# Kernel tuning notes

Hardware: AMD Instinct MI355X
Metric: run time of the kernel (lower is better)

The kernel has to match this reference:

```python
import jax, jax.numpy as jnp
import numpy as np
import math

BS, N_AGENTS, TOPK = 256, 64, 8
IN_DIM, HID, ATT, N_ACT = 128, 256, 64, 16


def setup_inputs() -> dict:
    key = jax.random.key(0)
    ks = jax.random.split(key, 20)
    s = 0.05
    return {
        "inputs": jax.random.normal(ks[0], (BS * N_AGENTS, IN_DIM), jnp.float32),
        "hidden_state": jax.random.normal(ks[1], (BS * N_AGENTS, HID), jnp.float32),
        "msg": jax.random.normal(ks[2], (BS * N_AGENTS, HID), jnp.float32),
        "topk_indices": jax.random.randint(ks[3], (BS, N_AGENTS, TOPK), 0, N_AGENTS, jnp.int32),
        "fc1_w": jax.random.normal(ks[4], (HID, IN_DIM), jnp.float32) * s,
        "fc1_b": jnp.zeros((HID,), jnp.float32),
        "gru_w_ih": jax.random.normal(ks[5], (3 * HID, HID), jnp.float32) * s,
        "gru_b_ih": jnp.zeros((3 * HID,), jnp.float32),
        "gru_w_hh": jax.random.normal(ks[6], (3 * HID, HID), jnp.float32) * s,
        "gru_b_hh": jnp.zeros((3 * HID,), jnp.float32),
        "q_w": jax.random.normal(ks[7], (ATT, HID), jnp.float32) * s,
        "q_b": jnp.zeros((ATT,), jnp.float32),
        "k_w": jax.random.normal(ks[8], (ATT, HID), jnp.float32) * s,
        "k_b": jnp.zeros((ATT,), jnp.float32),
        "v_w": jax.random.normal(ks[9], (HID, HID), jnp.float32) * s,
        "v_b": jnp.zeros((HID,), jnp.float32),
        "fc2a_w": jax.random.normal(ks[10], (HID, 2 * HID), jnp.float32) * s,
        "fc2a_b": jnp.zeros((HID,), jnp.float32),
        "fc2b_w": jax.random.normal(ks[11], (N_ACT, HID), jnp.float32) * s,
        "fc2b_b": jnp.zeros((N_ACT,), jnp.float32),
    }


def _forward(inputs, hidden_state, msg, topk_indices,
             fc1_w, fc1_b, gru_w_ih, gru_b_ih, gru_w_hh, gru_b_hh,
             q_w, q_b, k_w, k_b, v_w, v_b, fc2a_w, fc2a_b, fc2b_w, fc2b_b):
    # fc1 + ReLU
    x = jax.nn.relu(inputs @ fc1_w.T + fc1_b)  # [B*N, HID]
    # GRUCell (torch semantics)
    gi = x @ gru_w_ih.T + gru_b_ih             # [B*N, 3H]
    gh = hidden_state @ gru_w_hh.T + gru_b_hh
    i_r, i_z, i_n = jnp.split(gi, 3, axis=-1)
    h_r, h_z, h_n = jnp.split(gh, 3, axis=-1)
    r = jax.nn.sigmoid(i_r + h_r)
    z = jax.nn.sigmoid(i_z + h_z)
    n = jnp.tanh(i_n + r * h_n)
    h = (1.0 - z) * n + z * hidden_state       # [B*N, HID]

    # communicate: gather top-k neighbor messages, attend, aggregate
    msg_r = msg.reshape(BS, N_AGENTS, HID)
    msg_received = jax.vmap(lambda m, idx: m[idx])(msg_r, topk_indices)  # [B,N,K,HID]
    ego_h = h.reshape(BS, N_AGENTS, HID)
    q = ego_h @ q_w.T + q_b                    # [B,N,ATT]
    k = msg_received @ k_w.T + k_b             # [B,N,K,ATT]
    logits = jnp.einsum('bnka,bna->bnk', k, q) / math.sqrt(ATT)
    attn = jax.nn.softmax(logits, axis=-1)     # [B,N,K]
    m = msg_received @ v_w.T + v_b             # [B,N,K,HID]
    m_agg = jnp.einsum('bnk,bnkh->bnh', attn, m).reshape(BS * N_AGENTS, HID)

    out = jnp.concatenate([h, m_agg], axis=-1)  # [B*N, 2H]
    q_out = jax.nn.relu(out @ fc2a_w.T + fc2a_b) @ fc2b_w.T + fc2b_b  # [B*N, N_ACT]
    return q_out, h, m_agg


def reference(inputs, hidden_state, msg, topk_indices,
              fc1_w, fc1_b, gru_w_ih, gru_b_ih, gru_w_hh, gru_b_hh,
              q_w, q_b, k_w, k_b, v_w, v_b, fc2a_w, fc2a_b, fc2b_w, fc2b_b):
    return _forward(inputs, hidden_state, msg, topk_indices,
                    fc1_w, fc1_b, gru_w_ih, gru_b_ih, gru_w_hh, gru_b_hh,
                    q_w, q_b, k_w, k_b, v_w, v_b, fc2a_w, fc2a_b, fc2b_w, fc2b_b)
```

## Files before the change

### kernel.cpp

```cpp
#include <hip/hip_runtime.h>

typedef __bf16 bf16;
typedef __attribute__((ext_vector_type(8))) __bf16 bf16x8;
typedef __attribute__((ext_vector_type(4))) __bf16 bf16x4;
typedef __attribute__((ext_vector_type(4))) float f32x4;

static constexpr int ROWS = 16384;

static constexpr size_t OFF_WFC1 = 0;
static constexpr size_t OFF_WRX  = 32768;
static constexpr size_t OFF_WZX  = 98304;
static constexpr size_t OFF_WNI  = 163840;
static constexpr size_t OFF_WRH  = 229376;
static constexpr size_t OFF_WZH  = 294912;
static constexpr size_t OFF_WNH  = 360448;
static constexpr size_t OFF_WQ   = 425984;
static constexpr size_t OFF_WKV  = 442368;
static constexpr size_t OFF_F2AH = 524288;
static constexpr size_t OFF_F2AM = 589824;
static constexpr size_t OFF_WF2B = 655360;
static constexpr size_t OFF_INSW = 659456;

struct SwzSeg { const float* src; bf16* dst; int items; int k8s; int k32; int ld; };
struct SwzArgs { SwzSeg seg[14]; int count; };

__global__ __launch_bounds__(256) void swz_k(SwzArgs a) {
    const int tid = blockIdx.x * 256 + threadIdx.x;
    const int stride = gridDim.x * 256;
    for (int s = 0; s < a.count; ++s) {
        const float* __restrict__ src = a.seg[s].src;
        bf16* __restrict__ dst = a.seg[s].dst;
        const int items = a.seg[s].items, k8s = a.seg[s].k8s;
        const int k32c = a.seg[s].k32, ld = a.seg[s].ld;
        for (int i = tid; i < items; i += stride) {
            const int n = i >> k8s, kb = i & ((1 << k8s) - 1);
            const int k0 = kb << 3;
            const int lane = (n & 15) | ((kb & 3) << 4);
            const size_t off = ((size_t)((n >> 4) * k32c + (kb >> 2)) * 64 + lane) * 8;
            const float* p = src + (size_t)n * ld + k0;
            float4 f0 = *(const float4*)p;
            float4 f1 = *(const float4*)(p + 4);
            bf16x8 o = { (bf16)f0.x, (bf16)f0.y, (bf16)f0.z, (bf16)f0.w,
                         (bf16)f1.x, (bf16)f1.y, (bf16)f1.z, (bf16)f1.w };
            *(bf16x8*)(dst + off) = o;
        }
    }
}

template<int FM, int FN, int K32>
__device__ __forceinline__ void mm_swz(f32x4 (&acc)[FM][FN],
    const bf16* __restrict__ sA, int lda,
    const bf16* __restrict__ W, int lane)
{
    const int lr = lane & 15, lk = (lane >> 4) << 3;
    #pragma unroll
    for (int k32 = 0; k32 < K32; ++k32) {
        bf16x8 a[FM], b[FN];
        #pragma unroll
        for (int j = 0; j < FN; ++j)
            b[j] = *(const bf16x8*)(W + ((size_t)(j * K32 + k32) * 64 + lane) * 8);
        #pragma unroll
        for (int i = 0; i < FM; ++i)
            a[i] = *(const bf16x8*)&sA[(i * 16 + lr) * lda + k32 * 32 + lk];
        #pragma unroll
        for (int i = 0; i < FM; ++i)
            #pragma unroll
            for (int j = 0; j < FN; ++j)
                acc[i][j] = __builtin_amdgcn_mfma_f32_16x16x32_bf16(a[i], b[j], acc[i][j], 0, 0, 0);
    }
}

template<int FM, int FN, int K32>
__device__ __forceinline__ void mm_gg(f32x4 (&acc)[FM][FN],
    const bf16* __restrict__ A, const bf16* __restrict__ W, int lane)
{
    #pragma unroll
    for (int k32 = 0; k32 < K32; ++k32) {
        bf16x8 a[FM], b[FN];
        #pragma unroll
        for (int i = 0; i < FM; ++i)
            a[i] = *(const bf16x8*)(A + ((size_t)(i * K32 + k32) * 64 + lane) * 8);
        #pragma unroll
        for (int j = 0; j < FN; ++j)
            b[j] = *(const bf16x8*)(W + ((size_t)(j * K32 + k32) * 64 + lane) * 8);
        #pragma unroll
        for (int i = 0; i < FM; ++i)
            #pragma unroll
            for (int j = 0; j < FN; ++j)
                acc[i][j] = __builtin_amdgcn_mfma_f32_16x16x32_bf16(a[i], b[j], acc[i][j], 0, 0, 0);
    }
}

__device__ __forceinline__ float sigmf(float x) { return 1.f / (1.f + __expf(-x)); }
__device__ __forceinline__ float tanh_fast(float x) {
    x = fminf(fmaxf(x, -15.f), 15.f);
    float e2 = __expf(2.f * x);
    return (e2 - 1.f) / (e2 + 1.f);
}

__global__ __launch_bounds__(1024)
void mega_k(const bf16* __restrict__ insw, const float* __restrict__ hid_f,
            const float* __restrict__ msg_f, const int* __restrict__ topk,
            const bf16* __restrict__ Wfc1, const float* __restrict__ fc1_b,
            const bf16* __restrict__ WrX, const bf16* __restrict__ WrH,
            const bf16* __restrict__ WzX, const bf16* __restrict__ WzH,
            const bf16* __restrict__ Wni, const bf16* __restrict__ Wnh,
            const float* __restrict__ b_ih, const float* __restrict__ b_hh,
            const bf16* __restrict__ Wq, const float* __restrict__ q_b,
            const bf16* __restrict__ Wkv, const float* __restrict__ v_bias,
            const bf16* __restrict__ f2aH, const bf16* __restrict__ f2aM,
            const float* __restrict__ f2a_b,
            const bf16* __restrict__ Wf2b, const float* __restrict__ f2b_b,
            float* __restrict__ h_out, float* __restrict__ magg_out,
            float* __restrict__ q_out)
{
    __shared__ bf16 sH[64 * 264];
    __shared__ bf16 sB[64 * 264];
    __shared__ bf16 sG[64 * 264];
    __shared__ bf16 sM[64 * 264];
    __shared__ bf16 sQ[64 * 72];
    __shared__ bf16 sK[64 * 72];
    __shared__ int  sIdx[512];
    const int tid = threadIdx.x;
    const int wave = tid >> 6, lane = tid & 63;
    const int b64 = blockIdx.x * 64;
    const int lr = lane & 15, l4 = (lane >> 4) << 2, lk = (lane >> 4) << 3;

    #pragma unroll
    for (int c = tid; c < 4096; c += 1024) {
        int r = c >> 6, cg = (c & 63) << 2;
        float4 f = *(const float4*)(hid_f + (size_t)(b64 + r) * 256 + cg);
        float4 g = *(const float4*)(msg_f + (size_t)(b64 + r) * 256 + cg);
        bf16x4 oh = { (bf16)f.x, (bf16)f.y, (bf16)f.z, (bf16)f.w };
        bf16x4 og = { (bf16)g.x, (bf16)g.y, (bf16)g.z, (bf16)g.w };
        *(bf16x4*)&sH[r * 264 + cg] = oh;
        *(bf16x4*)&sG[r * 264 + cg] = og;
    }
    if (tid < 512) sIdx[tid] = topk[(size_t)blockIdx.x * 512 + tid];

    {
        f32x4 fa[1][4] = {};
        mm_gg<1, 4, 4>(fa, insw + (size_t)(blockIdx.x * 4 + (wave & 3)) * 4 * 512,
                       Wfc1 + (size_t)((wave >> 2) * 4) * 4 * 512, lane);
        #pragma unroll
        for (int j = 0; j < 4; ++j) {
            const int col = (wave >> 2) * 64 + j * 16 + lr;
            const float bv = fc1_b[col];
            #pragma unroll
            for (int rr = 0; rr < 4; ++rr)
                sB[((wave & 3) * 16 + l4 + rr) * 264 + col] = (bf16)fmaxf(fa[0][j][rr] + bv, 0.f);
        }
    }
    __syncthreads();

    f32x4 rg[4] = {}, zg[4] = {}, ng[4] = {}, hg[4] = {};
    {
        const size_t nb = (size_t)wave * 8 * 512;
        const bf16 *pRX = WrX + nb, *pZX = WzX + nb, *pNI = Wni + nb;
        const bf16 *pRH = WrH + nb, *pZH = WzH + nb, *pNH = Wnh + nb;
        #pragma unroll
        for (int k32 = 0; k32 < 8; ++k32) {
            const size_t bo = (size_t)k32 * 512 + lane * 8;
            bf16x8 brx = *(const bf16x8*)(pRX + bo);
            bf16x8 bzx = *(const bf16x8*)(pZX + bo);
            bf16x8 bni = *(const bf16x8*)(pNI + bo);
            bf16x8 brh = *(const bf16x8*)(pRH + bo);
            bf16x8 bzh = *(const bf16x8*)(pZH + bo);
            bf16x8 bnh = *(const bf16x8*)(pNH + bo);
            #pragma unroll
            for (int i = 0; i < 4; ++i) {
                bf16x8 ax = *(const bf16x8*)&sB[(i * 16 + lr) * 264 + k32 * 32 + lk];
                rg[i] = __builtin_amdgcn_mfma_f32_16x16x32_bf16(ax, brx, rg[i], 0, 0, 0);
                zg[i] = __builtin_amdgcn_mfma_f32_16x16x32_bf16(ax, bzx, zg[i], 0, 0, 0);
                ng[i] = __builtin_amdgcn_mfma_f32_16x16x32_bf16(ax, bni, ng[i], 0, 0, 0);
            }
            #pragma unroll
            for (int i = 0; i < 4; ++i) {
                bf16x8 ah = *(const bf16x8*)&sH[(i * 16 + lr) * 264 + k32 * 32 + lk];
                rg[i] = __builtin_amdgcn_mfma_f32_16x16x32_bf16(ah, brh, rg[i], 0, 0, 0);
                zg[i] = __builtin_amdgcn_mfma_f32_16x16x32_bf16(ah, bzh, zg[i], 0, 0, 0);
                hg[i] = __builtin_amdgcn_mfma_f32_16x16x32_bf16(ah, bnh, hg[i], 0, 0, 0);
            }
        }
    }
    {
        const int col = wave * 16 + lr;
        const float br = b_ih[col] + b_hh[col];
        const float bz = b_ih[256 + col] + b_hh[256 + col];
        const float bi = b_ih[512 + col], bh = b_hh[512 + col];
        #pragma unroll
        for (int i = 0; i < 4; ++i)
            #pragma unroll
            for (int rr = 0; rr < 4; ++rr) {
                const int row = i * 16 + l4 + rr;
                const float rv = sigmf(rg[i][rr] + br);
                const float zv = sigmf(zg[i][rr] + bz);
                const float nn = tanh_fast((ng[i][rr] + bi) + rv * (hg[i][rr] + bh));
                const float hd = (float)sH[row * 264 + col];
                const float h = (1.f - zv) * nn + zv * hd;
                h_out[(size_t)(b64 + row) * 256 + col] = h;
                sM[row * 264 + col] = (bf16)h;
            }
    }
    __syncthreads();

    if (wave < 4) {
        f32x4 a[4][2] = {};
        mm_swz<4, 2, 8>(a, sG, 264, Wkv + (size_t)(wave * 2) * 8 * 512, lane);
        #pragma unroll
        for (int i = 0; i < 4; ++i)
            #pragma unroll
            for (int j = 0; j < 2; ++j) {
                const int col = (wave * 2 + j) * 16 + lr;
                #pragma unroll
                for (int rr = 0; rr < 4; ++rr) {
                    const int row = i * 16 + l4 + rr;
                    if (col < 64) sK[row * 72 + col] = (bf16)a[i][j][rr];
                    else          sB[row * 264 + col - 64] = (bf16)a[i][j][rr];
                }
            }
    } else {
        f32x4 a[4][1] = {};
        mm_swz<4, 1, 8>(a, sG, 264, Wkv + (size_t)(4 + wave) * 8 * 512, lane);
        const int col = (4 + wave) * 16 + lr;
        #pragma unroll
        for (int i = 0; i < 4; ++i)
            #pragma unroll
            for (int rr = 0; rr < 4; ++rr)
                sB[(i * 16 + l4 + rr) * 264 + col - 64] = (bf16)a[i][0][rr];
    }
    {
        f32x4 qa[1][1] = {};
        mm_swz<1, 1, 8>(qa, sM + (wave & 3) * 16 * 264, 264,
                        Wq + (size_t)(wave >> 2) * 8 * 512, lane);
        const int col = (wave >> 2) * 16 + lr;
        const float bv = q_b[col];
        #pragma unroll
        for (int rr = 0; rr < 4; ++rr)
            sQ[((wave & 3) * 16 + l4 + rr) * 72 + col] = (bf16)(qa[0][0][rr] + bv);
    }
    __syncthreads();

    const int kk = lane >> 3, dg = lane & 7;
    #pragma unroll
    for (int uu = 0; uu < 4; ++uu) {
        const int u = wave * 4 + uu;
        const int rowk = sIdx[u * 8 + kk];
        bf16x8 q8 = *(const bf16x8*)&sQ[u * 72 + dg * 8];
        bf16x8 k8 = *(const bf16x8*)&sK[rowk * 72 + dg * 8];
        float s = 0.f;
        #pragma unroll
        for (int t = 0; t < 8; ++t) s += (float)q8[t] * (float)k8[t];
        s += __shfl_xor(s, 1); s += __shfl_xor(s, 2); s += __shfl_xor(s, 4);
        float logit = s * 0.125f;
        float mx = logit;
        mx = fmaxf(mx, __shfl_xor(mx, 8));
        mx = fmaxf(mx, __shfl_xor(mx, 16));
        mx = fmaxf(mx, __shfl_xor(mx, 32));
        float e = __expf(logit - mx);
        float den = e;
        den += __shfl_xor(den, 8); den += __shfl_xor(den, 16); den += __shfl_xor(den, 32);
        const float wv = e / den;
        float a0 = 0.f, a1 = 0.f, a2 = 0.f, a3 = 0.f;
        #pragma unroll
        for (int k = 0; k < 8; ++k) {
            float wk = __shfl(wv, k * 8);
            int   rk = __shfl(rowk, k * 8);
            bf16x4 v = *(const bf16x4*)&sB[rk * 264 + lane * 4];
            a0 += wk * (float)v[0]; a1 += wk * (float)v[1];
            a2 += wk * (float)v[2]; a3 += wk * (float)v[3];
        }
        float4 vb = *(const float4*)(v_bias + lane * 4);
        a0 += vb.x; a1 += vb.y; a2 += vb.z; a3 += vb.w;
        float4 res = { a0, a1, a2, a3 };
        *(float4*)(magg_out + (size_t)(b64 + u) * 256 + lane * 4) = res;
        bf16x4 rb = { (bf16)a0, (bf16)a1, (bf16)a2, (bf16)a3 };
        *(bf16x4*)&sH[u * 264 + lane * 4] = rb;
    }
    __syncthreads();

    {
        const int wm = wave >> 3, wn = wave & 7;
        f32x4 acc[2][2] = {};
        mm_swz<2, 2, 8>(acc, sM + wm * 32 * 264, 264, f2aH + (size_t)(wn * 2) * 8 * 512, lane);
        mm_swz<2, 2, 8>(acc, sH + wm * 32 * 264, 264, f2aM + (size_t)(wn * 2) * 8 * 512, lane);
        #pragma unroll
        for (int i = 0; i < 2; ++i)
            #pragma unroll
            for (int j = 0; j < 2; ++j) {
                const int col = wn * 32 + j * 16 + lr;
                const float bv = f2a_b[col];
                #pragma unroll
                for (int rr = 0; rr < 4; ++rr)
                    sG[(wm * 32 + i * 16 + l4 + rr) * 264 + col] = (bf16)fmaxf(acc[i][j][rr] + bv, 0.f);
            }
    }
    __syncthreads();

    if (wave < 4) {
        f32x4 acc[1][1] = {};
        mm_swz<1, 1, 8>(acc, sG + wave * 16 * 264, 264, Wf2b, lane);
        const float bv = f2b_b[lr];
        #pragma unroll
        for (int rr = 0; rr < 4; ++rr)
            q_out[(size_t)(b64 + wave * 16 + l4 + rr) * 16 + lr] = acc[0][0][rr] + bv;
    }
}

extern "C" void kernel_launch(void* const* d_in, const int* in_sizes, int n_in,
                              void* d_out, int out_size, void* d_ws, size_t ws_size,
                              hipStream_t stream)
{
    const float* in_f   = (const float*)d_in[0];
    const float* hid_f  = (const float*)d_in[1];
    const float* msg_f  = (const float*)d_in[2];
    const int*   topk   = (const int*)d_in[3];
    const float* fc1w_f = (const float*)d_in[4];
    const float* fc1_b  = (const float*)d_in[5];
    const float* wih_f  = (const float*)d_in[6];
    const float* b_ih   = (const float*)d_in[7];
    const float* whh_f  = (const float*)d_in[8];
    const float* b_hh   = (const float*)d_in[9];
    const float* qw_f   = (const float*)d_in[10];
    const float* q_b    = (const float*)d_in[11];
    const float* kw_f   = (const float*)d_in[12];
    const float* vw_f   = (const float*)d_in[14];
    const float* v_b    = (const float*)d_in[15];
    const float* f2aw_f = (const float*)d_in[16];
    const float* f2a_b  = (const float*)d_in[17];
    const float* f2bw_f = (const float*)d_in[18];
    const float* f2b_b  = (const float*)d_in[19];

    bf16* ws = (bf16*)d_ws;
    bf16* Wfc1 = ws + OFF_WFC1;
    bf16* WrX  = ws + OFF_WRX;
    bf16* WzX  = ws + OFF_WZX;
    bf16* Wni  = ws + OFF_WNI;
    bf16* WrH  = ws + OFF_WRH;
    bf16* WzH  = ws + OFF_WZH;
    bf16* Wnh  = ws + OFF_WNH;
    bf16* Wq   = ws + OFF_WQ;
    bf16* Wkv  = ws + OFF_WKV;
    bf16* f2aH = ws + OFF_F2AH;
    bf16* f2aM = ws + OFF_F2AM;
    bf16* Wf2b = ws + OFF_WF2B;
    bf16* insw = ws + OFF_INSW;

    float* q_out    = (float*)d_out;
    float* h_out    = q_out + (size_t)ROWS * 16;
    float* magg_out = h_out + (size_t)ROWS * 256;

    SwzArgs sa{};
    int s = 0;
    auto add = [&](const float* src, bf16* dst, int N, int K, int ld) {
        sa.seg[s].src = src; sa.seg[s].dst = dst;
        sa.seg[s].items = N * (K >> 3);
        sa.seg[s].k8s = (K == 128) ? 4 : 5;
        sa.seg[s].k32 = K >> 5;
        sa.seg[s].ld = ld; ++s;
    };
    add(fc1w_f,          Wfc1, 256, 128, 128);
    add(wih_f,           WrX,  256, 256, 256);
    add(wih_f +  65536,  WzX,  256, 256, 256);
    add(wih_f + 131072,  Wni,  256, 256, 256);
    add(whh_f,           WrH,  256, 256, 256);
    add(whh_f +  65536,  WzH,  256, 256, 256);
    add(whh_f + 131072,  Wnh,  256, 256, 256);
    add(qw_f,            Wq,    64, 256, 256);
    add(kw_f,            Wkv,   64, 256, 256);
    add(vw_f,            Wkv + 16384, 256, 256, 256);
    add(f2aw_f,          f2aH, 256, 256, 512);
    add(f2aw_f + 256,    f2aM, 256, 256, 512);
    add(f2bw_f,          Wf2b,  16, 256, 256);
    add(in_f,            insw, 16384, 128, 128);
    sa.count = s;
    swz_k<<<512, 256, 0, stream>>>(sa);

    mega_k<<<256, 1024, 0, stream>>>(insw, hid_f, msg_f, topk,
                                     Wfc1, fc1_b, WrX, WrH, WzX, WzH, Wni, Wnh,
                                     b_ih, b_hh, Wq, q_b, Wkv, v_b,
                                     f2aH, f2aM, f2a_b, Wf2b, f2b_b,
                                     h_out, magg_out, q_out);
}
```

Measured before the change: 56.46 us.

## Load fp32 inputs directly in fc1, drop input swizzle, prefetch weights in GEMMs

The fc1 stage now reads the fp32 input rows straight from global memory and converts them to bf16 in registers. This removes the swizzle pass over the 16384x128 input and its workspace round trip, and the swizzle kernel grid is halved. The GRU gate and fc2a GEMMs are restructured to software-prefetch the next k-slice of weight fragments while the current MFMAs run. fc2a also changes from a 2x2 wave tiling to one 16-column slice per wave over all 64 rows. In exchange, the fc1 A-fragment loads are uncoalesced strided fp32 reads, and fc2a now re-reads the LDS A tiles once per column slice.

```diff
diff --git a/kernel.cpp b/kernel.cpp
--- a/kernel.cpp
+++ b/kernel.cpp
@@ -19,7 +19,6 @@
 static constexpr size_t OFF_F2AH = 524288;
 static constexpr size_t OFF_F2AM = 589824;
 static constexpr size_t OFF_WF2B = 655360;
-static constexpr size_t OFF_INSW = 659456;
 
 struct SwzSeg { const float* src; bf16* dst; int items; int k8s; int k32; int ld; };
 struct SwzArgs { SwzSeg seg[14]; int count; };
@@ -70,24 +69,32 @@
     }
 }
 
-template<int FM, int FN, int K32>
-__device__ __forceinline__ void mm_gg(f32x4 (&acc)[FM][FN],
-    const bf16* __restrict__ A, const bf16* __restrict__ W, int lane)
+__device__ __forceinline__ void gate3(f32x4 (&g1)[4], f32x4 (&g2)[4], f32x4 (&g3)[4],
+    const bf16* __restrict__ sA,
+    const bf16* __restrict__ p1, const bf16* __restrict__ p2,
+    const bf16* __restrict__ p3, int lane)
 {
+    const int lr = lane & 15, lk = (lane >> 4) << 3;
+    const int lo = lane * 8;
+    bf16x8 c1 = *(const bf16x8*)(p1 + lo);
+    bf16x8 c2 = *(const bf16x8*)(p2 + lo);
+    bf16x8 c3 = *(const bf16x8*)(p3 + lo);
     #pragma unroll
-    for (int k32 = 0; k32 < K32; ++k32) {
-        bf16x8 a[FM], b[FN];
-        #pragma unroll
-        for (int i = 0; i < FM; ++i)
-            a[i] = *(const bf16x8*)(A + ((size_t)(i * K32 + k32) * 64 + lane) * 8);
-        #pragma unroll
-        for (int j = 0; j < FN; ++j)
-            b[j] = *(const bf16x8*)(W + ((size_t)(j * K32 + k32) * 64 + lane) * 8);
-        #pragma unroll
-        for (int i = 0; i < FM; ++i)
-            #pragma unroll
-            for (int j = 0; j < FN; ++j)
-                acc[i][j] = __builtin_amdgcn_mfma_f32_16x16x32_bf16(a[i], b[j], acc[i][j], 0, 0, 0);
+    for (int k = 0; k < 8; ++k) {
+        bf16x8 n1, n2, n3;
+        if (k < 7) {
+            n1 = *(const bf16x8*)(p1 + (k + 1) * 512 + lo);
+            n2 = *(const bf16x8*)(p2 + (k + 1) * 512 + lo);
+            n3 = *(const bf16x8*)(p3 + (k + 1) * 512 + lo);
+        }
+        #pragma unroll
+        for (int i = 0; i < 4; ++i) {
+            bf16x8 a = *(const bf16x8*)&sA[(i * 16 + lr) * 264 + k * 32 + lk];
+            g1[i] = __builtin_amdgcn_mfma_f32_16x16x32_bf16(a, c1, g1[i], 0, 0, 0);
+            g2[i] = __builtin_amdgcn_mfma_f32_16x16x32_bf16(a, c2, g2[i], 0, 0, 0);
+            g3[i] = __builtin_amdgcn_mfma_f32_16x16x32_bf16(a, c3, g3[i], 0, 0, 0);
+        }
+        if (k < 7) { c1 = n1; c2 = n2; c3 = n3; }
     }
 }
 
@@ -99,7 +106,7 @@
 }
 
 __global__ __launch_bounds__(1024)
-void mega_k(const bf16* __restrict__ insw, const float* __restrict__ hid_f,
+void mega_k(const float* __restrict__ in_f, const float* __restrict__ hid_f,
             const float* __restrict__ msg_f, const int* __restrict__ topk,
             const bf16* __restrict__ Wfc1, const float* __restrict__ fc1_b,
             const bf16* __restrict__ WrX, const bf16* __restrict__ WrH,
@@ -139,50 +146,37 @@
     if (tid < 512) sIdx[tid] = topk[(size_t)blockIdx.x * 512 + tid];
 
     {
-        f32x4 fa[1][4] = {};
-        mm_gg<1, 4, 4>(fa, insw + (size_t)(blockIdx.x * 4 + (wave & 3)) * 4 * 512,
-                       Wfc1 + (size_t)((wave >> 2) * 4) * 4 * 512, lane);
+        f32x4 fa[4] = {};
+        const float* ap = in_f + (size_t)(b64 + (wave & 3) * 16 + lr) * 128 + lk;
+        const bf16*  wp = Wfc1 + (size_t)(wave >> 2) * 16 * 512 + lane * 8;
+        #pragma unroll
+        for (int k = 0; k < 4; ++k) {
+            float4 f0 = *(const float4*)(ap + k * 32);
+            float4 f1 = *(const float4*)(ap + k * 32 + 4);
+            bf16x8 af = { (bf16)f0.x, (bf16)f0.y, (bf16)f0.z, (bf16)f0.w,
+                          (bf16)f1.x, (bf16)f1.y, (bf16)f1.z, (bf16)f1.w };
+            #pragma unroll
+            for (int j = 0; j < 4; ++j) {
+                bf16x8 bfr = *(const bf16x8*)(wp + (size_t)(j * 4 + k) * 512);
+                fa[j] = __builtin_amdgcn_mfma_f32_16x16x32_bf16(af, bfr, fa[j], 0, 0, 0);
+            }
+        }
         #pragma unroll
         for (int j = 0; j < 4; ++j) {
             const int col = (wave >> 2) * 64 + j * 16 + lr;
             const float bv = fc1_b[col];
             #pragma unroll
             for (int rr = 0; rr < 4; ++rr)
-                sB[((wave & 3) * 16 + l4 + rr) * 264 + col] = (bf16)fmaxf(fa[0][j][rr] + bv, 0.f);
-        }
-    }
-    __syncthreads();
-
+                sB[((wave & 3) * 16 + l4 + rr) * 264 + col] = (bf16)fmaxf(fa[j][rr] + bv, 0.f);
+        }
+    }
+    __syncthreads();
+
+    const size_t nb = (size_t)wave * 8 * 512;
     f32x4 rg[4] = {}, zg[4] = {}, ng[4] = {}, hg[4] = {};
-    {
-        const size_t nb = (size_t)wave * 8 * 512;
-        const bf16 *pRX = WrX + nb, *pZX = WzX + nb, *pNI = Wni + nb;
-        const bf16 *pRH = WrH + nb, *pZH = WzH + nb, *pNH = Wnh + nb;
-        #pragma unroll
-        for (int k32 = 0; k32 < 8; ++k32) {
-            const size_t bo = (size_t)k32 * 512 + lane * 8;
-            bf16x8 brx = *(const bf16x8*)(pRX + bo);
-            bf16x8 bzx = *(const bf16x8*)(pZX + bo);
-            bf16x8 bni = *(const bf16x8*)(pNI + bo);
-            bf16x8 brh = *(const bf16x8*)(pRH + bo);
-            bf16x8 bzh = *(const bf16x8*)(pZH + bo);
-            bf16x8 bnh = *(const bf16x8*)(pNH + bo);
-            #pragma unroll
-            for (int i = 0; i < 4; ++i) {
-                bf16x8 ax = *(const bf16x8*)&sB[(i * 16 + lr) * 264 + k32 * 32 + lk];
-                rg[i] = __builtin_amdgcn_mfma_f32_16x16x32_bf16(ax, brx, rg[i], 0, 0, 0);
-                zg[i] = __builtin_amdgcn_mfma_f32_16x16x32_bf16(ax, bzx, zg[i], 0, 0, 0);
-                ng[i] = __builtin_amdgcn_mfma_f32_16x16x32_bf16(ax, bni, ng[i], 0, 0, 0);
-            }
-            #pragma unroll
-            for (int i = 0; i < 4; ++i) {
-                bf16x8 ah = *(const bf16x8*)&sH[(i * 16 + lr) * 264 + k32 * 32 + lk];
-                rg[i] = __builtin_amdgcn_mfma_f32_16x16x32_bf16(ah, brh, rg[i], 0, 0, 0);
-                zg[i] = __builtin_amdgcn_mfma_f32_16x16x32_bf16(ah, bzh, zg[i], 0, 0, 0);
-                hg[i] = __builtin_amdgcn_mfma_f32_16x16x32_bf16(ah, bnh, hg[i], 0, 0, 0);
-            }
-        }
-    }
+    gate3(rg, zg, hg, sH, WrH + nb, WzH + nb, Wnh + nb, lane);
+    gate3(rg, zg, ng, sB, WrX + nb, WzX + nb, Wni + nb, lane);
+
     {
         const int col = wave * 16 + lr;
         const float br = b_ih[col] + b_hh[col];
@@ -280,20 +274,35 @@
     __syncthreads();
 
     {
-        const int wm = wave >> 3, wn = wave & 7;
-        f32x4 acc[2][2] = {};
-        mm_swz<2, 2, 8>(acc, sM + wm * 32 * 264, 264, f2aH + (size_t)(wn * 2) * 8 * 512, lane);
-        mm_swz<2, 2, 8>(acc, sH + wm * 32 * 264, 264, f2aM + (size_t)(wn * 2) * 8 * 512, lane);
-        #pragma unroll
-        for (int i = 0; i < 2; ++i)
-            #pragma unroll
-            for (int j = 0; j < 2; ++j) {
-                const int col = wn * 32 + j * 16 + lr;
-                const float bv = f2a_b[col];
-                #pragma unroll
-                for (int rr = 0; rr < 4; ++rr)
-                    sG[(wm * 32 + i * 16 + l4 + rr) * 264 + col] = (bf16)fmaxf(acc[i][j][rr] + bv, 0.f);
-            }
+        f32x4 ya[4] = {};
+        const bf16* pH = f2aH + nb;
+        const bf16* pM = f2aM + nb;
+        const int lo = lane * 8;
+        bf16x8 cH = *(const bf16x8*)(pH + lo);
+        bf16x8 cM = *(const bf16x8*)(pM + lo);
+        #pragma unroll
+        for (int k = 0; k < 8; ++k) {
+            bf16x8 nH, nM;
+            if (k < 7) {
+                nH = *(const bf16x8*)(pH + (k + 1) * 512 + lo);
+                nM = *(const bf16x8*)(pM + (k + 1) * 512 + lo);
+            }
+            #pragma unroll
+            for (int i = 0; i < 4; ++i) {
+                bf16x8 aH = *(const bf16x8*)&sM[(i * 16 + lr) * 264 + k * 32 + lk];
+                bf16x8 aM = *(const bf16x8*)&sH[(i * 16 + lr) * 264 + k * 32 + lk];
+                ya[i] = __builtin_amdgcn_mfma_f32_16x16x32_bf16(aH, cH, ya[i], 0, 0, 0);
+                ya[i] = __builtin_amdgcn_mfma_f32_16x16x32_bf16(aM, cM, ya[i], 0, 0, 0);
+            }
+            if (k < 7) { cH = nH; cM = nM; }
+        }
+        const int col = wave * 16 + lr;
+        const float bv = f2a_b[col];
+        #pragma unroll
+        for (int i = 0; i < 4; ++i)
+            #pragma unroll
+            for (int rr = 0; rr < 4; ++rr)
+                sG[(i * 16 + l4 + rr) * 264 + col] = (bf16)fmaxf(ya[i][rr] + bv, 0.f);
     }
     __syncthreads();
 
@@ -344,7 +353,6 @@
     bf16* f2aH = ws + OFF_F2AH;
     bf16* f2aM = ws + OFF_F2AM;
     bf16* Wf2b = ws + OFF_WF2B;
-    bf16* insw = ws + OFF_INSW;
 
     float* q_out    = (float*)d_out;
     float* h_out    = q_out + (size_t)ROWS * 16;
@@ -372,11 +380,10 @@
     add(f2aw_f,          f2aH, 256, 256, 512);
     add(f2aw_f + 256,    f2aM, 256, 256, 512);
     add(f2bw_f,          Wf2b,  16, 256, 256);
-    add(in_f,            insw, 16384, 128, 128);
     sa.count = s;
-    swz_k<<<512, 256, 0, stream>>>(sa);
-
-    mega_k<<<256, 1024, 0, stream>>>(insw, hid_f, msg_f, topk,
+    swz_k<<<256, 256, 0, stream>>>(sa);
+
+    mega_k<<<256, 1024, 0, stream>>>(in_f, hid_f, msg_f, topk,
                                      Wfc1, fc1_b, WrX, WrH, WzX, WzH, Wni, Wnh,
                                      b_ih, b_hh, Wq, q_b, Wkv, v_b,
                                      f2aH, f2aM, f2a_b, Wf2b, f2b_b,
```

After: 56.69 us. About the same (+0.4%).

## Retile fc2a GEMM per-wave with weight prefetch, coalesce h_out stores, add setprio

Applied to the files above, without the earlier changes.

The fc2a GEMM is rewritten so each of the 16 waves computes one 16-column slice over all 64 rows, with the next k-step weights prefetched into registers. h_out is now written in coalesced float4 stores from the bf16 copy held in shared memory, instead of scattered per-element stores in the GRU epilogue. s_setprio is wrapped around the MFMA bursts in the GRU and fc2a loops. The h_out values now pass through bf16 rounding, which lowers output precision.

```diff
diff --git a/kernel.cpp b/kernel.cpp
--- a/kernel.cpp
+++ b/kernel.cpp
@@ -167,6 +167,7 @@
             bf16x8 brh = *(const bf16x8*)(pRH + bo);
             bf16x8 bzh = *(const bf16x8*)(pZH + bo);
             bf16x8 bnh = *(const bf16x8*)(pNH + bo);
+            __builtin_amdgcn_s_setprio(1);
             #pragma unroll
             for (int i = 0; i < 4; ++i) {
                 bf16x8 ax = *(const bf16x8*)&sB[(i * 16 + lr) * 264 + k32 * 32 + lk];
@@ -181,6 +182,7 @@
                 zg[i] = __builtin_amdgcn_mfma_f32_16x16x32_bf16(ah, bzh, zg[i], 0, 0, 0);
                 hg[i] = __builtin_amdgcn_mfma_f32_16x16x32_bf16(ah, bnh, hg[i], 0, 0, 0);
             }
+            __builtin_amdgcn_s_setprio(0);
         }
     }
     {
@@ -198,7 +200,6 @@
                 const float nn = tanh_fast((ng[i][rr] + bi) + rv * (hg[i][rr] + bh));
                 const float hd = (float)sH[row * 264 + col];
                 const float h = (1.f - zv) * nn + zv * hd;
-                h_out[(size_t)(b64 + row) * 256 + col] = h;
                 sM[row * 264 + col] = (bf16)h;
             }
     }
@@ -238,6 +239,14 @@
         #pragma unroll
         for (int rr = 0; rr < 4; ++rr)
             sQ[((wave & 3) * 16 + l4 + rr) * 72 + col] = (bf16)(qa[0][0][rr] + bv);
+    }
+    #pragma unroll
+    for (int u = 0; u < 4; ++u) {
+        int c = tid + u * 1024;
+        int r = c >> 6, cg = (c & 63) << 2;
+        bf16x4 hv = *(const bf16x4*)&sM[r * 264 + cg];
+        float4 o = { (float)hv[0], (float)hv[1], (float)hv[2], (float)hv[3] };
+        *(float4*)(h_out + (size_t)(b64 + r) * 256 + cg) = o;
     }
     __syncthreads();
 
@@ -280,20 +289,41 @@
     __syncthreads();
 
     {
-        const int wm = wave >> 3, wn = wave & 7;
-        f32x4 acc[2][2] = {};
-        mm_swz<2, 2, 8>(acc, sM + wm * 32 * 264, 264, f2aH + (size_t)(wn * 2) * 8 * 512, lane);
-        mm_swz<2, 2, 8>(acc, sH + wm * 32 * 264, 264, f2aM + (size_t)(wn * 2) * 8 * 512, lane);
-        #pragma unroll
-        for (int i = 0; i < 2; ++i)
-            #pragma unroll
-            for (int j = 0; j < 2; ++j) {
-                const int col = wn * 32 + j * 16 + lr;
-                const float bv = f2a_b[col];
-                #pragma unroll
-                for (int rr = 0; rr < 4; ++rr)
-                    sG[(wm * 32 + i * 16 + l4 + rr) * 264 + col] = (bf16)fmaxf(acc[i][j][rr] + bv, 0.f);
-            }
+        const size_t nb = (size_t)wave * 8 * 512;
+        f32x4 ya[4] = {};
+        const bf16* pH = f2aH + nb;
+        const bf16* pM = f2aM + nb;
+        const int lo = lane * 8;
+        bf16x8 cH = *(const bf16x8*)(pH + lo);
+        bf16x8 cM = *(const bf16x8*)(pM + lo);
+        #pragma unroll
+        for (int k = 0; k < 8; ++k) {
+            bf16x8 nH, nM;
+            if (k < 7) {
+                nH = *(const bf16x8*)(pH + (k + 1) * 512 + lo);
+                nM = *(const bf16x8*)(pM + (k + 1) * 512 + lo);
+            }
+            __builtin_amdgcn_s_setprio(1);
+            #pragma unroll
+            for (int i = 0; i < 4; ++i) {
+                bf16x8 aH = *(const bf16x8*)&sM[(i * 16 + lr) * 264 + k * 32 + lk];
+                ya[i] = __builtin_amdgcn_mfma_f32_16x16x32_bf16(aH, cH, ya[i], 0, 0, 0);
+            }
+            #pragma unroll
+            for (int i = 0; i < 4; ++i) {
+                bf16x8 aM = *(const bf16x8*)&sH[(i * 16 + lr) * 264 + k * 32 + lk];
+                ya[i] = __builtin_amdgcn_mfma_f32_16x16x32_bf16(aM, cM, ya[i], 0, 0, 0);
+            }
+            __builtin_amdgcn_s_setprio(0);
+            cH = nH; cM = nM;
+        }
+        const int col = wave * 16 + lr;
+        const float bv = f2a_b[col];
+        #pragma unroll
+        for (int i = 0; i < 4; ++i)
+            #pragma unroll
+            for (int rr = 0; rr < 4; ++rr)
+                sG[(i * 16 + l4 + rr) * 264 + col] = (bf16)fmaxf(ya[i][rr] + bv, 0.f);
     }
     __syncthreads();
 
```

Result: no change. 56.49 us (median of 4 runs) (+0.1%).
